# Performance work log

Measured on AMD Instinct MI355X. Metric: run time of the kernel, lower is better.

## Reference

```python
import jax, jax.numpy as jnp
import numpy as np

B, N, T, S = 1, 16, 2048, 2048
G, I = 1, 2
M = N // G  # heads per group


def setup_inputs() -> dict:
    key = jax.random.key(0)
    ks = jax.random.split(key, 8)
    return {
        "inputs": jax.random.normal(ks[0], (B, N, T, S), dtype=jnp.float32),
        "qw1": jax.random.normal(ks[1], (B, T, G, I, M), dtype=jnp.float32) * 0.05,
        "qw2": jax.random.normal(ks[2], (B, T, G, I, M), dtype=jnp.float32) * 0.05,
        "kw1": jax.random.normal(ks[3], (B, S, G, I, M), dtype=jnp.float32) * 0.05,
        "kw2": jax.random.normal(ks[4], (B, S, G, I, M), dtype=jnp.float32) * 0.05,
        "qdd": jax.random.normal(ks[5], (B, T, G, M), dtype=jnp.float32) * 0.05,
        "kdd": jax.random.normal(ks[6], (B, S, G, M), dtype=jnp.float32) * 0.05,
        "w": jax.random.normal(ks[7], (G, M, M), dtype=jnp.float32) * 0.02,
    }


def reference(inputs, qw1, qw2, kw1, kw2, qdd, kdd, w):
    b, n, t, s = inputs.shape
    g, m = w.shape[0], w.shape[1]
    x = inputs.reshape(b, g, m, t, s)  # BGMTS
    # static cross-head mixing (w + identity)
    wi = w + jnp.eye(m, dtype=w.dtype)
    ret = jnp.einsum('BGMTS,GMN->BGNTS', x, wi)
    # dynamic low-rank mixing, query-side (per T position); the original loops
    # over the I axis — summing over I is mathematically identical.
    hq = jnp.einsum('BGMTS,BTGIM->BGITS', x, qw1)
    ret = ret + jnp.einsum('BGITS,BTGIM->BGMTS', hq, qw2)
    # dynamic low-rank mixing, key-side (per S position)
    hk = jnp.einsum('BGMTS,BSGIM->BGITS', x, kw1)
    ret = ret + jnp.einsum('BGITS,BSGIM->BGMTS', hk, kw2)
    # dynamic diagonal terms
    ret = ret + jnp.einsum('BGMTS,BTGM->BGMTS', x, qdd)
    ret = ret + jnp.einsum('BGMTS,BSGM->BGMTS', x, kdd)
    return ret.reshape(b, n, t, s)
```

## Files before the change

### kernel.cpp

```cpp
#include <hip/hip_runtime.h>


#define TDIM 2048
#define SDIM 2048
#define TT 8
#define SBLK 256
#define THREADS 512

typedef float vf4 __attribute__((ext_vector_type(4)));

__device__ __forceinline__ void barrier_nodrain() {
  asm volatile("s_waitcnt lgkmcnt(0)" ::: "memory");
  __builtin_amdgcn_s_barrier();
  asm volatile("" ::: "memory");
}

__device__ __forceinline__ void pin4(vf4& v) {
  float a = v.x, b = v.y, c = v.z, d = v.w;
  asm volatile("" : "+v"(a), "+v"(b), "+v"(c), "+v"(d));
  v.x = a; v.y = b; v.z = c; v.w = d;
}

__global__ void chp_prep(const float* __restrict__ kw1, const float* __restrict__ kw2,
                         const float* __restrict__ kdd,
                         float* __restrict__ kt1, float* __restrict__ kt2,
                         float* __restrict__ kddt) {
  int tid = blockIdx.x * blockDim.x + threadIdx.x;
  if (tid < 65536) {
    int im = tid >> 11, s = tid & 2047;
    kt1[tid] = kw1[s * 32 + im];
  } else if (tid < 131072) {
    int v = tid - 65536;
    int im = v >> 11, s = v & 2047;
    kt2[v] = kw2[s * 32 + im];
  } else if (tid < 163840) {
    int v = tid - 131072;
    int n = v >> 11, s = v & 2047;
    kddt[v] = kdd[s * 16 + n];
  }
}

__device__ __forceinline__ vf4 ld4(const float* p) {
  return *reinterpret_cast<const vf4*>(p);
}
__device__ __forceinline__ vf4 ld4nt(const float* p) {
  return __builtin_nontemporal_load(reinterpret_cast<const vf4*>(p));
}
__device__ __forceinline__ void fma4(vf4& d, const vf4& a, const vf4& b) {
  d.x = fmaf(a.x, b.x, d.x); d.y = fmaf(a.y, b.y, d.y);
  d.z = fmaf(a.z, b.z, d.z); d.w = fmaf(a.w, b.w, d.w);
}
__device__ __forceinline__ void fma4s(vf4& d, const vf4& a, float b) {
  d.x = fmaf(a.x, b, d.x); d.y = fmaf(a.y, b, d.y);
  d.z = fmaf(a.z, b, d.z); d.w = fmaf(a.w, b, d.w);
}

template <bool KT>
__global__ __launch_bounds__(THREADS, 4) void chp_main(
    const float* __restrict__ in, const float* __restrict__ w,
    const float* __restrict__ qw1, const float* __restrict__ qw2,
    const float* __restrict__ qdd, const float* __restrict__ kw1,
    const float* __restrict__ kw2, const float* __restrict__ kdd,
    const float* __restrict__ kt1, const float* __restrict__ kt2,
    const float* __restrict__ kddt, float* __restrict__ out) {
  __shared__ vf4 x_lds[2][16][65];
  __shared__ float wq_lds[2][256];

  const int tid = threadIdx.x;
  const int wv = tid >> 6;
  const int lane = tid & 63;
  const int j = lane & 7;
  const int qg = lane >> 3;
  const int quad = wv * 8 + qg;
  const int s0 = blockIdx.x * SBLK + quad * 4;
  const int t0 = blockIdx.y * TT;

  vf4 kt1v[2][2], kt2v[2][2], kdv[2];
  if constexpr (KT) {
#pragma unroll
    for (int i = 0; i < 2; ++i)
#pragma unroll
      for (int k = 0; k < 2; ++k) {
        kt1v[i][k] = ld4(kt1 + (size_t)(i * 16 + 2 * j + k) * SDIM + s0);
        kt2v[i][k] = ld4(kt2 + (size_t)(i * 16 + 2 * j + k) * SDIM + s0);
      }
#pragma unroll
    for (int k = 0; k < 2; ++k) kdv[k] = ld4(kddt + (size_t)(2 * j + k) * SDIM + s0);
  } else {
#pragma unroll
    for (int i = 0; i < 2; ++i)
#pragma unroll
      for (int k = 0; k < 2; ++k)
#pragma unroll
        for (int c = 0; c < 4; ++c) {
          kt1v[i][k][c] = kw1[(size_t)(s0 + c) * 32 + i * 16 + 2 * j + k];
          kt2v[i][k][c] = kw2[(size_t)(s0 + c) * 32 + i * 16 + 2 * j + k];
        }
#pragma unroll
    for (int k = 0; k < 2; ++k)
#pragma unroll
      for (int c = 0; c < 4; ++c) kdv[k][c] = kdd[(size_t)(s0 + c) * 16 + 2 * j + k];
  }
#pragma unroll
  for (int i = 0; i < 2; ++i)
#pragma unroll
    for (int k = 0; k < 2; ++k) { pin4(kt1v[i][k]); pin4(kt2v[i][k]); }
#pragma unroll
  for (int k = 0; k < 2; ++k) pin4(kdv[k]);

  const bool builder = (tid < 256);
  const int bm = (tid >> 4) & 15, bn = tid & 15;
  const float wbase = builder ? w[bm * 16 + bn] : 0.0f;

  vf4 xp[2];
  float q1a = 0.f, q1b = 0.f, q2a = 0.f, q2b = 0.f, qd = 0.f;

  auto prefetch = [&](int t) {
#pragma unroll
    for (int k = 0; k < 2; ++k)
      xp[k] = ld4nt(in + ((size_t)(2 * j + k) * TDIM + t) * SDIM + s0);
    if (builder) {
      q1a = qw1[t * 32 + bm];
      q1b = qw1[t * 32 + 16 + bm];
      q2a = qw2[t * 32 + bn];
      q2b = qw2[t * 32 + 16 + bn];
      qd = qdd[t * 16 + bn];
    }
  };
  auto stage = [&](int buf) {
#pragma unroll
    for (int k = 0; k < 2; ++k) x_lds[buf][2 * j + k][quad] = xp[k];
    if (builder) {
      float v = fmaf(q1a, q2a, fmaf(q1b, q2b, wbase));
      if (bm == bn) v += 1.0f + qd;
      wq_lds[buf][tid] = v;
    }
  };

  prefetch(t0);
  stage(0);
  prefetch(t0 + 1);
  barrier_nodrain();

  int cur = 0;
  for (int tt = 0; tt < TT; ++tt) {
    const int t = t0 + tt;
    const int nxt = cur ^ 1;

    vf4 acc[2];
    vf4 p0 = (vf4){0.f, 0.f, 0.f, 0.f}, p1 = p0;
    acc[0] = (vf4){0.f, 0.f, 0.f, 0.f};
    acc[1] = (vf4){0.f, 0.f, 0.f, 0.f};

#pragma unroll
    for (int m = 0; m < 16; ++m) {
      const vf4 xm = x_lds[cur][m][quad];
      const float* wp = &wq_lds[cur][m * 16 + 2 * j];
      fma4s(acc[0], xm, wp[0]);
      fma4s(acc[1], xm, wp[1]);
      if ((m >> 1) == j) {
        const int k = m & 1;
        fma4(p0, xm, kt1v[0][k]);
        fma4(p1, xm, kt1v[1][k]);
        fma4(acc[k], xm, kdv[k]);
      }
    }
#pragma unroll
    for (int mask = 1; mask <= 4; mask <<= 1) {
      p0.x += __shfl_xor(p0.x, mask); p0.y += __shfl_xor(p0.y, mask);
      p0.z += __shfl_xor(p0.z, mask); p0.w += __shfl_xor(p0.w, mask);
      p1.x += __shfl_xor(p1.x, mask); p1.y += __shfl_xor(p1.y, mask);
      p1.z += __shfl_xor(p1.z, mask); p1.w += __shfl_xor(p1.w, mask);
    }
#pragma unroll
    for (int r = 0; r < 2; ++r) {
      fma4(acc[r], p0, kt2v[0][r]);
      fma4(acc[r], p1, kt2v[1][r]);
      *reinterpret_cast<vf4*>(out + ((size_t)(2 * j + r) * TDIM + t) * SDIM + s0) =
          acc[r];
    }

    if (tt + 1 < TT) {
      stage(nxt);
      if (tt + 2 < TT) prefetch(t + 2);
    }
    barrier_nodrain();
    cur = nxt;
  }
}

extern "C" void kernel_launch(void* const* d_in, const int* in_sizes, int n_in,
                              void* d_out, int out_size, void* d_ws, size_t ws_size,
                              hipStream_t stream) {
  const float* in = (const float*)d_in[0];
  const float* qw1 = (const float*)d_in[1];
  const float* qw2 = (const float*)d_in[2];
  const float* kw1 = (const float*)d_in[3];
  const float* kw2 = (const float*)d_in[4];
  const float* qdd = (const float*)d_in[5];
  const float* kdd = (const float*)d_in[6];
  const float* w = (const float*)d_in[7];
  float* out = (float*)d_out;
  float* ws = (float*)d_ws;

  const bool useKT = (ws_size >= 163840ull * sizeof(float));
  float* kt1 = ws;
  float* kt2 = ws + 65536;
  float* kddt = ws + 131072;

  dim3 grid(SDIM / SBLK, TDIM / TT);
  if (useKT) {
    hipLaunchKernelGGL(chp_prep, dim3(640), dim3(256), 0, stream, kw1, kw2, kdd, kt1,
                       kt2, kddt);
    hipLaunchKernelGGL((chp_main<true>), grid, dim3(THREADS), 0, stream, in, w, qw1,
                       qw2, qdd, kw1, kw2, kdd, kt1, kt2, kddt, out);
  } else {
    hipLaunchKernelGGL((chp_main<false>), grid, dim3(THREADS), 0, stream, in, w, qw1,
                       qw2, qdd, kw1, kw2, kdd, nullptr, nullptr, nullptr, out);
  }
}
```

Measured before the change: 140.4 us.

## Remap waves to head pairs and reduce key-side projection through LDS

```diff
diff --git a/kernel.cpp b/kernel.cpp
--- a/kernel.cpp
+++ b/kernel.cpp
@@ -8,6 +8,7 @@
 #define THREADS 512
 
 typedef float vf4 __attribute__((ext_vector_type(4)));
+typedef float vf2 __attribute__((ext_vector_type(2)));
 
 __device__ __forceinline__ void barrier_nodrain() {
   asm volatile("s_waitcnt lgkmcnt(0)" ::: "memory");
@@ -54,6 +55,9 @@
   d.x = fmaf(a.x, b, d.x); d.y = fmaf(a.y, b, d.y);
   d.z = fmaf(a.z, b, d.z); d.w = fmaf(a.w, b, d.w);
 }
+__device__ __forceinline__ void add4(vf4& d, const vf4& a) {
+  d.x += a.x; d.y += a.y; d.z += a.z; d.w += a.w;
+}
 
 template <bool KT>
 __global__ __launch_bounds__(THREADS, 4) void chp_main(
@@ -65,15 +69,14 @@
     const float* __restrict__ kddt, float* __restrict__ out) {
   __shared__ vf4 x_lds[2][16][65];
   __shared__ float wq_lds[2][256];
+  __shared__ vf4 hk_lds[8][2][64];
 
   const int tid = threadIdx.x;
   const int wv = tid >> 6;
   const int lane = tid & 63;
-  const int j = lane & 7;
-  const int qg = lane >> 3;
-  const int quad = wv * 8 + qg;
-  const int s0 = blockIdx.x * SBLK + quad * 4;
+  const int s0 = blockIdx.x * SBLK + lane * 4;
   const int t0 = blockIdx.y * TT;
+  const int r0 = 2 * wv;
 
   vf4 kt1v[2][2], kt2v[2][2], kdv[2];
   if constexpr (KT) {
@@ -81,11 +84,11 @@
     for (int i = 0; i < 2; ++i)
 #pragma unroll
       for (int k = 0; k < 2; ++k) {
-        kt1v[i][k] = ld4(kt1 + (size_t)(i * 16 + 2 * j + k) * SDIM + s0);
-        kt2v[i][k] = ld4(kt2 + (size_t)(i * 16 + 2 * j + k) * SDIM + s0);
+        kt1v[i][k] = ld4(kt1 + (size_t)(i * 16 + r0 + k) * SDIM + s0);
+        kt2v[i][k] = ld4(kt2 + (size_t)(i * 16 + r0 + k) * SDIM + s0);
       }
 #pragma unroll
-    for (int k = 0; k < 2; ++k) kdv[k] = ld4(kddt + (size_t)(2 * j + k) * SDIM + s0);
+    for (int k = 0; k < 2; ++k) kdv[k] = ld4(kddt + (size_t)(r0 + k) * SDIM + s0);
   } else {
 #pragma unroll
     for (int i = 0; i < 2; ++i)
@@ -93,13 +96,13 @@
       for (int k = 0; k < 2; ++k)
 #pragma unroll
         for (int c = 0; c < 4; ++c) {
-          kt1v[i][k][c] = kw1[(size_t)(s0 + c) * 32 + i * 16 + 2 * j + k];
-          kt2v[i][k][c] = kw2[(size_t)(s0 + c) * 32 + i * 16 + 2 * j + k];
+          kt1v[i][k][c] = kw1[(size_t)(s0 + c) * 32 + i * 16 + r0 + k];
+          kt2v[i][k][c] = kw2[(size_t)(s0 + c) * 32 + i * 16 + r0 + k];
         }
 #pragma unroll
     for (int k = 0; k < 2; ++k)
 #pragma unroll
-      for (int c = 0; c < 4; ++c) kdv[k][c] = kdd[(size_t)(s0 + c) * 16 + 2 * j + k];
+      for (int c = 0; c < 4; ++c) kdv[k][c] = kdd[(size_t)(s0 + c) * 16 + r0 + k];
   }
 #pragma unroll
   for (int i = 0; i < 2; ++i)
@@ -118,7 +121,7 @@
   auto prefetch = [&](int t) {
 #pragma unroll
     for (int k = 0; k < 2; ++k)
-      xp[k] = ld4nt(in + ((size_t)(2 * j + k) * TDIM + t) * SDIM + s0);
+      xp[k] = ld4nt(in + ((size_t)(r0 + k) * TDIM + t) * SDIM + s0);
     if (builder) {
       q1a = qw1[t * 32 + bm];
       q1b = qw1[t * 32 + 16 + bm];
@@ -129,7 +132,7 @@
   };
   auto stage = [&](int buf) {
 #pragma unroll
-    for (int k = 0; k < 2; ++k) x_lds[buf][2 * j + k][quad] = xp[k];
+    for (int k = 0; k < 2; ++k) x_lds[buf][r0 + k][lane] = xp[k];
     if (builder) {
       float v = fmaf(q1a, q2a, fmaf(q1b, q2b, wbase));
       if (bm == bn) v += 1.0f + qd;
@@ -148,35 +151,38 @@
     const int nxt = cur ^ 1;
 
     vf4 acc[2];
-    vf4 p0 = (vf4){0.f, 0.f, 0.f, 0.f}, p1 = p0;
+    vf4 pp0 = (vf4){0.f, 0.f, 0.f, 0.f}, pp1 = pp0;
     acc[0] = (vf4){0.f, 0.f, 0.f, 0.f};
     acc[1] = (vf4){0.f, 0.f, 0.f, 0.f};
 
 #pragma unroll
     for (int m = 0; m < 16; ++m) {
-      const vf4 xm = x_lds[cur][m][quad];
-      const float* wp = &wq_lds[cur][m * 16 + 2 * j];
-      fma4s(acc[0], xm, wp[0]);
-      fma4s(acc[1], xm, wp[1]);
-      if ((m >> 1) == j) {
+      const vf4 xm = x_lds[cur][m][lane];
+      const vf2 wp = *reinterpret_cast<const vf2*>(&wq_lds[cur][m * 16 + r0]);
+      fma4s(acc[0], xm, wp.x);
+      fma4s(acc[1], xm, wp.y);
+      if ((m >> 1) == wv) {
         const int k = m & 1;
-        fma4(p0, xm, kt1v[0][k]);
-        fma4(p1, xm, kt1v[1][k]);
+        fma4(pp0, xm, kt1v[0][k]);
+        fma4(pp1, xm, kt1v[1][k]);
         fma4(acc[k], xm, kdv[k]);
       }
     }
-#pragma unroll
-    for (int mask = 1; mask <= 4; mask <<= 1) {
-      p0.x += __shfl_xor(p0.x, mask); p0.y += __shfl_xor(p0.y, mask);
-      p0.z += __shfl_xor(p0.z, mask); p0.w += __shfl_xor(p0.w, mask);
-      p1.x += __shfl_xor(p1.x, mask); p1.y += __shfl_xor(p1.y, mask);
-      p1.z += __shfl_xor(p1.z, mask); p1.w += __shfl_xor(p1.w, mask);
+    hk_lds[wv][0][lane] = pp0;
+    hk_lds[wv][1][lane] = pp1;
+    barrier_nodrain();
+
+    vf4 hk0 = (vf4){0.f, 0.f, 0.f, 0.f}, hk1 = hk0;
+#pragma unroll
+    for (int wsrc = 0; wsrc < 8; ++wsrc) {
+      add4(hk0, hk_lds[wsrc][0][lane]);
+      add4(hk1, hk_lds[wsrc][1][lane]);
     }
 #pragma unroll
     for (int r = 0; r < 2; ++r) {
-      fma4(acc[r], p0, kt2v[0][r]);
-      fma4(acc[r], p1, kt2v[1][r]);
-      *reinterpret_cast<vf4*>(out + ((size_t)(2 * j + r) * TDIM + t) * SDIM + s0) =
+      fma4(acc[r], hk0, kt2v[0][r]);
+      fma4(acc[r], hk1, kt2v[1][r]);
+      *reinterpret_cast<vf4*>(out + ((size_t)(r0 + r) * TDIM + t) * SDIM + s0) =
           acc[r];
     }
 
```

Result: slower. 188.9 us (+34.5%).

## Make LDS staging wave-private to eliminate block-wide barriers

Applied to the files above, without the earlier changes.

```diff
diff --git a/kernel.cpp b/kernel.cpp
--- a/kernel.cpp
+++ b/kernel.cpp
@@ -8,12 +8,6 @@
 #define THREADS 512
 
 typedef float vf4 __attribute__((ext_vector_type(4)));
-
-__device__ __forceinline__ void barrier_nodrain() {
-  asm volatile("s_waitcnt lgkmcnt(0)" ::: "memory");
-  __builtin_amdgcn_s_barrier();
-  asm volatile("" ::: "memory");
-}
 
 __device__ __forceinline__ void pin4(vf4& v) {
   float a = v.x, b = v.y, c = v.z, d = v.w;
@@ -63,16 +57,15 @@
     const float* __restrict__ kw2, const float* __restrict__ kdd,
     const float* __restrict__ kt1, const float* __restrict__ kt2,
     const float* __restrict__ kddt, float* __restrict__ out) {
-  __shared__ vf4 x_lds[2][16][65];
-  __shared__ float wq_lds[2][256];
+  __shared__ vf4 x_lds[8][16][9];
+  __shared__ float wq_lds[8][256];
 
   const int tid = threadIdx.x;
   const int wv = tid >> 6;
   const int lane = tid & 63;
   const int j = lane & 7;
   const int qg = lane >> 3;
-  const int quad = wv * 8 + qg;
-  const int s0 = blockIdx.x * SBLK + quad * 4;
+  const int s0 = blockIdx.x * SBLK + wv * 32 + qg * 4;
   const int t0 = blockIdx.y * TT;
 
   vf4 kt1v[2][2], kt2v[2][2], kdv[2];
@@ -108,44 +101,42 @@
 #pragma unroll
   for (int k = 0; k < 2; ++k) pin4(kdv[k]);
 
-  const bool builder = (tid < 256);
-  const int bm = (tid >> 4) & 15, bn = tid & 15;
-  const float wbase = builder ? w[bm * 16 + bn] : 0.0f;
+  const int bm = lane >> 2;
+  const int bn0 = (lane & 3) * 4;
+  const vf4 wb4 = ld4(w + bm * 16 + bn0);
 
   vf4 xp[2];
-  float q1a = 0.f, q1b = 0.f, q2a = 0.f, q2b = 0.f, qd = 0.f;
+  float q1a = 0.f, q1b = 0.f;
+  vf4 q2a, q2b, qdv4;
 
   auto prefetch = [&](int t) {
 #pragma unroll
     for (int k = 0; k < 2; ++k)
       xp[k] = ld4nt(in + ((size_t)(2 * j + k) * TDIM + t) * SDIM + s0);
-    if (builder) {
-      q1a = qw1[t * 32 + bm];
-      q1b = qw1[t * 32 + 16 + bm];
-      q2a = qw2[t * 32 + bn];
-      q2b = qw2[t * 32 + 16 + bn];
-      qd = qdd[t * 16 + bn];
-    }
+    q1a = qw1[t * 32 + bm];
+    q1b = qw1[t * 32 + 16 + bm];
+    q2a = ld4(qw2 + t * 32 + bn0);
+    q2b = ld4(qw2 + t * 32 + 16 + bn0);
+    qdv4 = ld4(qdd + t * 16 + bn0);
   };
-  auto stage = [&](int buf) {
-#pragma unroll
-    for (int k = 0; k < 2; ++k) x_lds[buf][2 * j + k][quad] = xp[k];
-    if (builder) {
-      float v = fmaf(q1a, q2a, fmaf(q1b, q2b, wbase));
-      if (bm == bn) v += 1.0f + qd;
-      wq_lds[buf][tid] = v;
-    }
+  auto stage = [&]() {
+#pragma unroll
+    for (int k = 0; k < 2; ++k) x_lds[wv][2 * j + k][qg] = xp[k];
+    vf4 v;
+#pragma unroll
+    for (int c = 0; c < 4; ++c) {
+      v[c] = fmaf(q1a, q2a[c], fmaf(q1b, q2b[c], wb4[c]));
+      v[c] += (bm == bn0 + c) ? (1.0f + qdv4[c]) : 0.0f;
+    }
+    *reinterpret_cast<vf4*>(&wq_lds[wv][bm * 16 + bn0]) = v;
   };
 
   prefetch(t0);
-  stage(0);
+  stage();
   prefetch(t0 + 1);
-  barrier_nodrain();
-
-  int cur = 0;
+
   for (int tt = 0; tt < TT; ++tt) {
     const int t = t0 + tt;
-    const int nxt = cur ^ 1;
 
     vf4 acc[2];
     vf4 p0 = (vf4){0.f, 0.f, 0.f, 0.f}, p1 = p0;
@@ -154,8 +145,8 @@
 
 #pragma unroll
     for (int m = 0; m < 16; ++m) {
-      const vf4 xm = x_lds[cur][m][quad];
-      const float* wp = &wq_lds[cur][m * 16 + 2 * j];
+      const vf4 xm = x_lds[wv][m][qg];
+      const float* wp = &wq_lds[wv][m * 16 + 2 * j];
       fma4s(acc[0], xm, wp[0]);
       fma4s(acc[1], xm, wp[1]);
       if ((m >> 1) == j) {
@@ -181,11 +172,9 @@
     }
 
     if (tt + 1 < TT) {
-      stage(nxt);
+      stage();
       if (tt + 2 < TT) prefetch(t + 2);
     }
-    barrier_nodrain();
-    cur = nxt;
   }
 }
 
```

After: 139.9 us. About the same (-0.4%).
